# Kernel optimization log

Hardware: AMD Instinct MI355X
Metric: run time of the kernel (lower is better)

## Reference

```python
import jax, jax.numpy as jnp
import numpy as np

# ---- module constants (from init_kwargs) ----
OUT_C = 64
NY, NX = 256, 256
PC = (-51.2, -51.2, -5.0, 51.2, 51.2, 3.0)  # xmin,ymin,zmin,xmax,ymax,zmax
VX, VY = 0.4, 0.4
DBINS, DMIN, DMAX = 16, 1.0, 60.0
SIGMA, MIN_OP, EPS = 0.8, 0.05, 1e-6

# 3x3 Gaussian kernel (radius=1, min_weight=0 keeps all 9 taps)
_offs = [(dy, dx) for dy in range(-1, 2) for dx in range(-1, 2)]
OFF_DY = jnp.array([o[0] for o in _offs], jnp.int32)
OFF_DX = jnp.array([o[1] for o in _offs], jnp.int32)
KW = jnp.array([np.exp(-(dx * dx + dy * dy) / (2.0 * SIGMA * SIGMA)) for dy, dx in _offs], jnp.float32)


def _conv(x, w, stride, pad):
    return jax.lax.conv_general_dilated(
        x, w, (stride, stride), [(pad, pad), (pad, pad)],
        dimension_numbers=('NCHW', 'OIHW', 'NCHW'))


def _cbr(x, w, s, b, stride):
    # conv + (eval-mode BN folded into scale/shift) + relu
    y = _conv(x, w, stride, 1)
    return jax.nn.relu(y * s[None, :, None, None] + b[None, :, None, None])


def _forward(images, cam_K, T_lc, w1, s1, b1, w2, s2, b2, w3, s3, b3, w4, s4, b4,
             fw1, fs1, fb1, fw2, fbias2, dw, dbias, ow, obias, img_h, img_w):
    x = _cbr(images, w1, s1, b1, 2)
    x = _cbr(x, w2, s2, b2, 2)
    x = _cbr(x, w3, s3, b3, 2)
    x4 = _cbr(x, w4, s4, b4, 2)                       # (B,128,Hf,Wf)
    fh = _cbr(x4, fw1, fs1, fb1, 1)
    features = _conv(fh, fw2, 1, 0) + fbias2[None, :, None, None]   # (B,C,Hf,Wf)
    depth_logits = _conv(x4, dw, 1, 0) + dbias[None, :, None, None]  # (B,D,Hf,Wf)
    opacity = jax.nn.sigmoid(_conv(x4, ow, 1, 0) + obias[None, :, None, None])[:, 0]  # (B,Hf,Wf)

    B, C, Hf, Wf = features.shape
    # lift_mode='expected': single depth hypothesis = E[depth] under softmax
    dprob = jax.nn.softmax(depth_logits, axis=1)
    dvals = jnp.linspace(DMIN, DMAX, DBINS, dtype=jnp.float32)
    z = jnp.einsum('bdhw,d->bhw', dprob, dvals)       # (B,Hf,Wf)

    # backproject feature-grid pixel centers to lidar frame
    ys = (jnp.arange(Hf, dtype=jnp.float32) + 0.5) * (float(img_h) / Hf)
    xs = (jnp.arange(Wf, dtype=jnp.float32) + 0.5) * (float(img_w) / Wf)
    yy, xx = jnp.meshgrid(ys, xs, indexing='ij')      # (Hf,Wf)
    fx = jnp.maximum(cam_K[:, 0, 0], EPS)[:, None, None]
    fy = jnp.maximum(cam_K[:, 1, 1], EPS)[:, None, None]
    cx = cam_K[:, 0, 2][:, None, None]
    cy = cam_K[:, 1, 2][:, None, None]
    x_cam = (xx[None] - cx) * z / fx
    y_cam = (yy[None] - cy) * z / fy
    pts = jnp.stack([x_cam, y_cam, z, jnp.ones_like(z)], axis=-1).reshape(B, -1, 4)
    lidar = jnp.einsum('bij,bnj->bni', T_lc, pts)[..., :3]   # (B,N,3)

    xw, yw, zw = lidar[..., 0], lidar[..., 1], lidar[..., 2]
    xi = jnp.floor((xw - PC[0]) / VX).astype(jnp.int32)
    yi = jnp.floor((yw - PC[1]) / VY).astype(jnp.int32)
    inb = (xi >= 0) & (xi < NX) & (yi >= 0) & (yi < NY) & (zw >= PC[2]) & (zw < PC[5])

    op = opacity.reshape(B, -1)
    base_w = op * (op >= MIN_OP) * inb                # invalid points -> zero weight

    N = Hf * Wf
    bidx = jnp.repeat(jnp.arange(B, dtype=jnp.int32), N)
    xi, yi = xi.reshape(-1), yi.reshape(-1)
    base_w = base_w.reshape(-1)
    feats = features.transpose(0, 2, 3, 1).reshape(-1, C)   # (B*N, C)
    S = NY * NX

    # vectorized Gaussian splat over the 9 kernel taps (no python loop over points)
    tx = xi[None, :] + OFF_DX[:, None]                # (9, B*N)
    ty = yi[None, :] + OFF_DY[:, None]
    vm = (tx >= 0) & (tx < NX) & (ty >= 0) & (ty < NY)
    sw = base_w[None, :] * KW[:, None] * vm           # scatter weights, 0 where invalid
    idx = jnp.where(vm, bidx[None, :] * S + ty * NX + tx, 0).reshape(-1)

    canvas = jnp.zeros((B * S, C), feats.dtype).at[idx].add((feats[None] * sw[..., None]).reshape(-1, C))
    wacc = jnp.zeros((B * S,), feats.dtype).at[idx].add(sw.reshape(-1))

    canvas = canvas / jnp.maximum(wacc, EPS)[:, None] * (wacc > 0)[:, None]
    return canvas.reshape(B, NY, NX, C).transpose(0, 3, 1, 2)   # (B,C,NY,NX)


def setup_inputs() -> dict:
    key = jax.random.key(0)
    ks = jax.random.split(key, 30)
    B, H, W = 4, 1024, 1536

    def he(k, shape, fan):
        return jax.random.normal(k, shape, jnp.float32) * np.float32(np.sqrt(2.0 / fan))

    def bn(k, c):
        k1, k2 = jax.random.split(k)
        return (1.0 + 0.1 * jax.random.normal(k1, (c,), jnp.float32),
                0.1 * jax.random.normal(k2, (c,), jnp.float32))

    inp = {}
    inp['images'] = jax.random.normal(ks[0], (B, 3, H, W), jnp.float32)

    K = np.zeros((B, 3, 3), np.float32)
    K[:, 0, 0] = 1200.0; K[:, 1, 1] = 1200.0
    K[:, 0, 2] = W / 2.0; K[:, 1, 2] = H / 2.0; K[:, 2, 2] = 1.0
    inp['cam_K'] = jnp.asarray(K)

    T = np.zeros((B, 4, 4), np.float32)
    T[:, :3, :3] = np.array([[0, 0, 1], [-1, 0, 0], [0, -1, 0]], np.float32)  # cam z -> lidar x
    T[:, 0, 3] = 0.5; T[:, 2, 3] = 1.6; T[:, 3, 3] = 1.0
    inp['T_lc'] = jnp.asarray(T)

    inp['w1'] = he(ks[1], (32, 3, 3, 3), 3 * 9);    inp['s1'], inp['b1'] = bn(ks[2], 32)
    inp['w2'] = he(ks[3], (64, 32, 3, 3), 32 * 9);  inp['s2'], inp['b2'] = bn(ks[4], 64)
    inp['w3'] = he(ks[5], (128, 64, 3, 3), 64 * 9); inp['s3'], inp['b3'] = bn(ks[6], 128)
    inp['w4'] = he(ks[7], (128, 128, 3, 3), 128 * 9); inp['s4'], inp['b4'] = bn(ks[8], 128)
    inp['fw1'] = he(ks[9], (128, 128, 3, 3), 128 * 9); inp['fs1'], inp['fb1'] = bn(ks[10], 128)
    inp['fw2'] = he(ks[11], (64, 128, 1, 1), 128)
    inp['fbias2'] = 0.01 * jax.random.normal(ks[12], (64,), jnp.float32)
    inp['dw'] = he(ks[13], (16, 128, 1, 1), 128)
    inp['dbias'] = 0.5 * jax.random.normal(ks[14], (16,), jnp.float32)
    inp['ow'] = he(ks[15], (1, 128, 1, 1), 128)
    inp['obias'] = jnp.full((1,), 0.5, jnp.float32)
    inp['img_h'] = 1024
    inp['img_w'] = 1536
    return inp


def reference(images, cam_K, T_lc, w1, s1, b1, w2, s2, b2, w3, s3, b3, w4, s4, b4,
              fw1, fs1, fb1, fw2, fbias2, dw, dbias, ow, obias, img_h, img_w):
    return _forward(images, cam_K, T_lc, w1, s1, b1, w2, s2, b2, w3, s3, b3, w4, s4, b4,
                    fw1, fs1, fb1, fw2, fbias2, dw, dbias, ow, obias, img_h, img_w)
```

## Files before the change

### kernel.cpp

```cpp
#include <hip/hip_runtime.h>
#include <math.h>


template<int STRIDE, int BANDS>
__global__ __launch_bounds__(256) void conv3x3_bn(
    const float* __restrict__ in, const float* __restrict__ wgt,
    const float* __restrict__ scl, const float* __restrict__ sft,
    float* __restrict__ out,
    int IC, int IH, int IW, int OC, int OH, int OW) {
  __shared__ float wl[1152];
  int chw = (OH * OW) >> 8;
  int spb = chw / (8 * BANDS);
  int x = blockIdx.x & 7;
  int y = blockIdx.x >> 3;
  int per_b = OC * chw;
  int ypb = per_b >> 3;
  int bb = y / ypb;
  int rem = y % ypb;
  int bandq = rem / (spb * OC);
  int rem2 = rem % (spb * OC);
  int s_loc = rem2 / OC;
  int oc_r = rem2 % OC;
  int s = (x * BANDS + bandq) * spb + s_loc;
  int chunk = bb * per_b + oc_r * chw + s;
  int idx = chunk * 256 + threadIdx.x;
  int ox = idx % OW;
  int tmp = idx / OW;
  int oy = tmp % OH;
  tmp /= OH;
  int oc = tmp % OC;
  int b = tmp / OC;
  int wn = IC * 9;
  for (int i = threadIdx.x; i < wn; i += 256) wl[i] = wgt[oc * wn + i];
  __syncthreads();

  const float* ip0 = in + (b * IC) * IH * IW;
  int iy0 = oy * STRIDE - 1;
  int ix0 = ox * STRIDE - 1;
  int plane = IH * IW;
  float acc = 0.f;
  if (iy0 >= 0 && iy0 + 2 < IH && ix0 >= 0 && ix0 + 2 < IW) {
    const float* ip = ip0 + iy0 * IW + ix0;
    const float* wp = wl;
    for (int ic = 0; ic < IC; ++ic) {
#pragma unroll
      for (int ky = 0; ky < 3; ++ky) {
        const float* r = ip + ky * IW;
        acc += r[0] * wp[ky * 3 + 0];
        acc += r[1] * wp[ky * 3 + 1];
        acc += r[2] * wp[ky * 3 + 2];
      }
      ip += plane;
      wp += 9;
    }
  } else {
    for (int ic = 0; ic < IC; ++ic) {
      const float* ip = ip0 + ic * plane;
      const float* wp = wl + ic * 9;
#pragma unroll
      for (int ky = 0; ky < 3; ++ky) {
        int iy = iy0 + ky;
        if (iy < 0 || iy >= IH) continue;
#pragma unroll
        for (int kx = 0; kx < 3; ++kx) {
          int ix = ix0 + kx;
          if (ix < 0 || ix >= IW) continue;
          acc += ip[iy * IW + ix] * wp[ky * 3 + kx];
        }
      }
    }
  }
  float r = acc * scl[oc] + sft[oc];
  out[idx] = r > 0.f ? r : 0.f;
}

template<int STRIDE, int IC, int OCB, int OCT, int NOC4, int TY, int TX>
__global__ __launch_bounds__(256) void conv3x3_t(
    const float* __restrict__ in, const float* __restrict__ wgt,
    const float* __restrict__ scl, const float* __restrict__ sft,
    float* __restrict__ out, int IH, int IW, int OH, int OW) {
  constexpr int OCG = NOC4 * 4;
  constexpr int NOCG = OCB / OCG;
  constexpr int NPIX_T = 256 / NOCG;
  constexpr int PIX = (TY * TX) / NPIX_T;
  constexpr int PH = (TY - 1) * STRIDE + 3;
  constexpr int PW = (TX - 1) * STRIDE + 3;
  __shared__ float patch[PH * PW];
  __shared__ float wl[9 * OCB];

  int NTY = OH / TY, NTX = OW / TX;
  int ntiles = 4 * NTY * NTX;
  int ocs = blockIdx.x / ntiles;
  int r = blockIdx.x % ntiles;
  int b = r / (NTY * NTX);
  int t = r % (NTY * NTX);
  int tyi = t / NTX, txi = t % NTX;
  int oc_base = ocs * OCB;

  int tid = threadIdx.x;
  int pid = tid % NPIX_T;
  int ocg = tid / NPIX_T;

  int off[PIX], pyv[PIX], pxv[PIX];
#pragma unroll
  for (int i = 0; i < PIX; ++i) {
    int p = i * NPIX_T + pid;
    pyv[i] = p / TX;
    pxv[i] = p % TX;
    off[i] = (pyv[i] * STRIDE) * PW + pxv[i] * STRIDE;
  }

  float4 acc[PIX][NOC4];
#pragma unroll
  for (int i = 0; i < PIX; ++i)
#pragma unroll
    for (int j = 0; j < NOC4; ++j) acc[i][j] = make_float4(0.f, 0.f, 0.f, 0.f);

  const size_t plane_in = (size_t)IH * IW;
  const float* ibase = in + (size_t)b * IC * plane_in;
  int iy0 = tyi * TY * STRIDE - 1;
  int ix0 = txi * TX * STRIDE - 1;

#pragma unroll 1
  for (int ic = 0; ic < IC; ++ic) {
    const float* ip = ibase + (size_t)ic * plane_in;
    for (int i = tid; i < PH * PW; i += 256) {
      int py = i / PW, px = i % PW;
      int iy = iy0 + py, ix = ix0 + px;
      float v = 0.f;
      if (iy >= 0 && iy < IH && ix >= 0 && ix < IW) v = ip[(size_t)iy * IW + ix];
      patch[i] = v;
    }
    for (int i = tid; i < 9 * OCB; i += 256) {
      int oc = i / 9, k = i % 9;
      wl[k * OCB + oc] = wgt[((size_t)(oc_base + oc) * IC + ic) * 9 + k];
    }
    __syncthreads();

    const float4* wl4 = (const float4*)wl;
#pragma unroll
    for (int ky = 0; ky < 3; ++ky) {
#pragma unroll
      for (int kx = 0; kx < 3; ++kx) {
        float pv[PIX];
#pragma unroll
        for (int i = 0; i < PIX; ++i) pv[i] = patch[off[i] + ky * PW + kx];
        const float4* wr = wl4 + (ky * 3 + kx) * (OCB / 4) + ocg * NOC4;
#pragma unroll
        for (int j = 0; j < NOC4; ++j) {
          float4 w = wr[j];
#pragma unroll
          for (int i = 0; i < PIX; ++i) {
            acc[i][j].x = __builtin_fmaf(pv[i], w.x, acc[i][j].x);
            acc[i][j].y = __builtin_fmaf(pv[i], w.y, acc[i][j].y);
            acc[i][j].z = __builtin_fmaf(pv[i], w.z, acc[i][j].z);
            acc[i][j].w = __builtin_fmaf(pv[i], w.w, acc[i][j].w);
          }
        }
      }
    }
    __syncthreads();
  }

  int plane = OH * OW;
#pragma unroll
  for (int i = 0; i < PIX; ++i) {
    int oy = tyi * TY + pyv[i];
    int ox = txi * TX + pxv[i];
#pragma unroll
    for (int j = 0; j < NOC4; ++j) {
      int oc0 = oc_base + ocg * OCG + j * 4;
      float4 v = acc[i][j];
      float4 sc = ((const float4*)scl)[oc0 >> 2];
      float4 sh = ((const float4*)sft)[oc0 >> 2];
      float rx = __builtin_fmaf(v.x, sc.x, sh.x);
      float ry = __builtin_fmaf(v.y, sc.y, sh.y);
      float rz = __builtin_fmaf(v.z, sc.z, sh.z);
      float rw = __builtin_fmaf(v.w, sc.w, sh.w);
      rx = rx > 0.f ? rx : 0.f;
      ry = ry > 0.f ? ry : 0.f;
      rz = rz > 0.f ? rz : 0.f;
      rw = rw > 0.f ? rw : 0.f;
      size_t base = ((size_t)b * OCT + oc0) * plane + oy * OW + ox;
      out[base] = rx;
      out[base + plane] = ry;
      out[base + 2 * (size_t)plane] = rz;
      out[base + 3 * (size_t)plane] = rw;
    }
  }
}

__global__ __launch_bounds__(256) void feat_head(
    const float* __restrict__ fh, const float* __restrict__ fw2,
    const float* __restrict__ fb, float* __restrict__ feats) {
  __shared__ float wl[128 * 64];
  for (int i = threadIdx.x; i < 8192; i += 256) {
    int c = i & 63, ic = i >> 6;
    wl[i] = fw2[c * 128 + ic];
  }
  __syncthreads();
  int t = blockIdx.x * 256 + threadIdx.x;
  int c = t & 63;
  int p = t >> 6;
  int b = p / 6144;
  int rem = p % 6144;
  const float* fp = fh + (b * 128) * 6144 + rem;
  float acc = fb[c];
#pragma unroll 4
  for (int ic = 0; ic < 128; ++ic) acc += fp[ic * 6144] * wl[(ic << 6) + c];
  feats[t] = acc;
}

__global__ __launch_bounds__(256) void depth_head(
    const float* __restrict__ x4, const float* __restrict__ dw,
    const float* __restrict__ dbias, const float* __restrict__ oww,
    const float* __restrict__ obias, const float* __restrict__ camK,
    const float* __restrict__ Tlc,
    int* __restrict__ xio, int* __restrict__ yio, float* __restrict__ bwo) {
  __shared__ float dwl[16 * 128];
  __shared__ float owl[128];
  for (int i = threadIdx.x; i < 2048; i += 256) dwl[i] = dw[i];
  if (threadIdx.x < 128) owl[threadIdx.x] = oww[threadIdx.x];
  __syncthreads();
  int p = blockIdx.x * 256 + threadIdx.x;
  int b = p / 6144;
  int rem = p % 6144;
  int y = rem / 96;
  int x = rem % 96;

  float lg[16];
#pragma unroll
  for (int j = 0; j < 16; ++j) lg[j] = dbias[j];
  float oa = obias[0];
  const float* fp = x4 + (b * 128) * 6144 + rem;
  for (int ic = 0; ic < 128; ++ic) {
    float f = fp[ic * 6144];
#pragma unroll
    for (int j = 0; j < 16; ++j) lg[j] += f * dwl[j * 128 + ic];
    oa += f * owl[ic];
  }
  float m = lg[0];
#pragma unroll
  for (int j = 1; j < 16; ++j) m = fmaxf(m, lg[j]);
  float se = 0.f, sz = 0.f;
#pragma unroll
  for (int j = 0; j < 16; ++j) {
    float e = expf(lg[j] - m);
    se += e;
    sz += e * (1.0f + (float)j * (59.0f / 15.0f));
  }
  float z = sz / se;
  float op = 1.f / (1.f + expf(-oa));

  const float* K = camK + b * 9;
  float fx = fmaxf(K[0], 1e-6f), fy = fmaxf(K[4], 1e-6f);
  float cx = K[2], cy = K[5];
  float xs = ((float)x + 0.5f) * 16.0f;
  float ys = ((float)y + 0.5f) * 16.0f;
  float xc = (xs - cx) * z / fx;
  float yc = (ys - cy) * z / fy;
  const float* T = Tlc + b * 16;
  float xw = T[0] * xc + T[1] * yc + T[2] * z + T[3];
  float yw = T[4] * xc + T[5] * yc + T[6] * z + T[7];
  float zw = T[8] * xc + T[9] * yc + T[10] * z + T[11];
  float xif = floorf((xw - (-51.2f)) / 0.4f);
  float yif = floorf((yw - (-51.2f)) / 0.4f);
  int xi = (int)xif, yi = (int)yif;
  bool inb = xi >= 0 && xi < 256 && yi >= 0 && yi < 256 && zw >= -5.0f && zw < 3.0f;
  float bw = (op >= 0.05f && inb) ? op : 0.f;
  xio[p] = xi;
  yio[p] = yi;
  bwo[p] = bw;
}

__global__ __launch_bounds__(256) void zerof4(float4* __restrict__ p) {
  int i = blockIdx.x * 256 + threadIdx.x;
  p[i] = make_float4(0.f, 0.f, 0.f, 0.f);
}

__global__ __launch_bounds__(256) void splat(
    const float* __restrict__ feats, const int* __restrict__ xi,
    const int* __restrict__ yi, const float* __restrict__ bw,
    float* __restrict__ canvas, float* __restrict__ wacc) {
  int t = blockIdx.x * 256 + threadIdx.x;
  int c = t & 63;
  int p = t >> 6;
  float w0 = bw[p];
  if (w0 == 0.f) return;
  int X = xi[p], Y = yi[p];
  int b = p / 6144;
  float fv = feats[t];
  float* cb = canvas + ((size_t)b << 22);
  float* wb = wacc + (b << 16);
  const float kwt[3] = {1.0f, 0.45783335f, 0.20961137f};
#pragma unroll
  for (int dy = -1; dy <= 1; ++dy) {
    int ty = Y + dy;
    if (ty < 0 || ty > 255) continue;
#pragma unroll
    for (int dx = -1; dx <= 1; ++dx) {
      int tx = X + dx;
      if (tx < 0 || tx > 255) continue;
      float kw = kwt[dx * dx + dy * dy];
      atomicAdd(&cb[(((ty << 8) + tx) << 6) + c], fv * w0 * kw);
      if (c == 0) atomicAdd(&wb[(ty << 8) + tx], w0 * kw);
    }
  }
}

__global__ __launch_bounds__(256) void normalize_out(
    const float* __restrict__ canvas, const float* __restrict__ wacc,
    float* __restrict__ out) {
  __shared__ float tile[64][65];
  int blk = blockIdx.x;
  int b = blk >> 10;
  int s0 = (blk & 1023) << 6;
  int tid = threadIdx.x;
  const float* cb = canvas + ((size_t)b << 22);
  const float* wb = wacc + (b << 16);
#pragma unroll
  for (int it = 0; it < 16; ++it) {
    int l = it * 256 + tid;
    int pix = l >> 6, ch = l & 63;
    float w = wb[s0 + pix];
    float n = w > 0.f ? 1.f / fmaxf(w, 1e-6f) : 0.f;
    tile[pix][ch] = cb[(size_t)(s0 + pix) * 64 + ch] * n;
  }
  __syncthreads();
  float* ob = out + ((size_t)b << 22);
#pragma unroll
  for (int it = 0; it < 16; ++it) {
    int l = it * 256 + tid;
    int ch = l >> 6, pix = l & 63;
    ob[(size_t)ch * 65536 + s0 + pix] = tile[pix][ch];
  }
}

extern "C" void kernel_launch(void* const* d_in, const int* in_sizes, int n_in,
                              void* d_out, int out_size, void* d_ws, size_t ws_size,
                              hipStream_t stream) {
  const float* images = (const float*)d_in[0];
  const float* camK   = (const float*)d_in[1];
  const float* Tlc    = (const float*)d_in[2];
  const float* w1 = (const float*)d_in[3];
  const float* s1 = (const float*)d_in[4];
  const float* b1 = (const float*)d_in[5];
  const float* w2 = (const float*)d_in[6];
  const float* s2 = (const float*)d_in[7];
  const float* b2 = (const float*)d_in[8];
  const float* w3 = (const float*)d_in[9];
  const float* s3 = (const float*)d_in[10];
  const float* b3 = (const float*)d_in[11];
  const float* w4 = (const float*)d_in[12];
  const float* s4 = (const float*)d_in[13];
  const float* b4 = (const float*)d_in[14];
  const float* fw1 = (const float*)d_in[15];
  const float* fs1 = (const float*)d_in[16];
  const float* fb1 = (const float*)d_in[17];
  const float* fw2 = (const float*)d_in[18];
  const float* fbias2 = (const float*)d_in[19];
  const float* dw = (const float*)d_in[20];
  const float* dbias = (const float*)d_in[21];
  const float* ow = (const float*)d_in[22];
  const float* obias = (const float*)d_in[23];
  float* out = (float*)d_out;

  float* ws = (float*)d_ws;
  float* A = ws;
  float* Bb = ws + 50331648;
  float* c4   = Bb;
  float* fhb  = Bb + 3145728;
  float* ftb  = Bb + 6291456;
  int*   xib  = (int*)(Bb + 7864320);
  int*   yib  = xib + 24576;
  float* bwb  = (float*)(yib + 24576);
  float* canvas = A;
  float* waccb  = A + 16777216;

  conv3x3_bn<2, 4><<<196608, 256, 0, stream>>>(images, w1, s1, b1, A, 3, 1024, 1536, 32, 512, 768);
  conv3x3_bn<2, 2><<<98304, 256, 0, stream>>>(A, w2, s2, b2, Bb, 32, 512, 768, 64, 256, 384);
  conv3x3_t<2, 64, 64, 128, 8, 8, 32><<<768, 256, 0, stream>>>(
      Bb, w3, s3, b3, A, 256, 384, 128, 192);
  conv3x3_t<2, 128, 32, 128, 4, 8, 16><<<768, 256, 0, stream>>>(
      A, w4, s4, b4, c4, 128, 192, 64, 96);
  conv3x3_t<1, 128, 32, 128, 4, 8, 16><<<768, 256, 0, stream>>>(
      c4, fw1, fs1, fb1, fhb, 64, 96, 64, 96);
  feat_head<<<6144, 256, 0, stream>>>(fhb, fw2, fbias2, ftb);
  depth_head<<<96, 256, 0, stream>>>(c4, dw, dbias, ow, obias, camK, Tlc, xib, yib, bwb);
  zerof4<<<16640, 256, 0, stream>>>((float4*)canvas);
  splat<<<6144, 256, 0, stream>>>(ftb, xib, yib, bwb, canvas, waccb);
  normalize_out<<<4096, 256, 0, stream>>>(canvas, waccb, out);
}
```

Measured before the change: 3.091 ms.

## Interleave conv1 and conv2 in four row-band chunks for cache locality

```diff
diff --git a/kernel.cpp b/kernel.cpp
--- a/kernel.cpp
+++ b/kernel.cpp
@@ -2,27 +2,22 @@
 #include <math.h>
 
 
-template<int STRIDE, int BANDS>
-__global__ __launch_bounds__(256) void conv3x3_bn(
+template<int STRIDE, int OCL2, int SPG>
+__global__ __launch_bounds__(256) void conv3x3_chunk(
     const float* __restrict__ in, const float* __restrict__ wgt,
     const float* __restrict__ scl, const float* __restrict__ sft,
     float* __restrict__ out,
-    int IC, int IH, int IW, int OC, int OH, int OW) {
+    int IC, int IH, int IW, int OC, int OH, int OW, int k) {
   __shared__ float wl[1152];
   int chw = (OH * OW) >> 8;
-  int spb = chw / (8 * BANDS);
   int x = blockIdx.x & 7;
   int y = blockIdx.x >> 3;
-  int per_b = OC * chw;
-  int ypb = per_b >> 3;
-  int bb = y / ypb;
-  int rem = y % ypb;
-  int bandq = rem / (spb * OC);
-  int rem2 = rem % (spb * OC);
-  int s_loc = rem2 / OC;
-  int oc_r = rem2 % OC;
-  int s = (x * BANDS + bandq) * spb + s_loc;
-  int chunk = bb * per_b + oc_r * chw + s;
+  int b_sel = x >> 1;
+  int g = x & 1;
+  int oc_r = y & ((1 << OCL2) - 1);
+  int s_loc = y >> OCL2;
+  int s = k * (2 * SPG) + g * SPG + s_loc;
+  int chunk = (b_sel * OC + oc_r) * chw + s;
   int idx = chunk * 256 + threadIdx.x;
   int ox = idx % OW;
   int tmp = idx / OW;
@@ -132,8 +127,8 @@
       patch[i] = v;
     }
     for (int i = tid; i < 9 * OCB; i += 256) {
-      int oc = i / 9, k = i % 9;
-      wl[k * OCB + oc] = wgt[((size_t)(oc_base + oc) * IC + ic) * 9 + k];
+      int oc = i / 9, kk = i % 9;
+      wl[kk * OCB + oc] = wgt[((size_t)(oc_base + oc) * IC + ic) * 9 + kk];
     }
     __syncthreads();
 
@@ -377,8 +372,12 @@
   float* canvas = A;
   float* waccb  = A + 16777216;
 
-  conv3x3_bn<2, 4><<<196608, 256, 0, stream>>>(images, w1, s1, b1, A, 3, 1024, 1536, 32, 512, 768);
-  conv3x3_bn<2, 2><<<98304, 256, 0, stream>>>(A, w2, s2, b2, Bb, 32, 512, 768, 64, 256, 384);
+  for (int k = 0; k < 4; ++k) {
+    conv3x3_chunk<2, 5, 192><<<49152, 256, 0, stream>>>(
+        images, w1, s1, b1, A, 3, 1024, 1536, 32, 512, 768, k);
+    conv3x3_chunk<2, 6, 48><<<24576, 256, 0, stream>>>(
+        A, w2, s2, b2, Bb, 32, 512, 768, 64, 256, 384, k);
+  }
   conv3x3_t<2, 64, 64, 128, 8, 8, 32><<<768, 256, 0, stream>>>(
       Bb, w3, s3, b3, A, 256, 384, 128, 192);
   conv3x3_t<2, 128, 32, 128, 4, 8, 16><<<768, 256, 0, stream>>>(
```

New measurement: 2.829 ms. 1.09x faster.
